# Performance work log

Hardware: AMD Instinct MI355X
Metric: run time of the kernel (lower is better)

The kernel has to match this reference:

```python
import jax, jax.numpy as jnp
import numpy as np
import math

D_MODEL = 1024
N_HEADS = 16
D_K = D_MODEL // N_HEADS
D_FF = 4096
B = 2
S = 2048
LN_EPS = 1e-3  # Keras LayerNormalization default


def setup_inputs() -> dict:
    key = jax.random.key(0)
    ks = jax.random.split(key, 16)
    s = 0.02
    inp = {
        "x": jax.random.normal(ks[0], (B, S, D_MODEL), dtype=jnp.float32),
        "weights": jax.random.uniform(ks[1], (B, S), dtype=jnp.float32),
        # attention projections (Dense: y = x @ W + b)
        "Wq": jax.random.normal(ks[2], (D_MODEL, D_MODEL), jnp.float32) * s,
        "bq": jnp.zeros((D_MODEL,), jnp.float32),
        "Wk": jax.random.normal(ks[3], (D_MODEL, D_MODEL), jnp.float32) * s,
        "bk": jnp.zeros((D_MODEL,), jnp.float32),
        "Wv": jax.random.normal(ks[4], (D_MODEL, D_MODEL), jnp.float32) * s,
        "bv": jnp.zeros((D_MODEL,), jnp.float32),
        "Wo": jax.random.normal(ks[5], (D_MODEL, D_MODEL), jnp.float32) * s,
        "bo": jnp.zeros((D_MODEL,), jnp.float32),
        # FFN
        "W1": jax.random.normal(ks[6], (D_MODEL, D_FF), jnp.float32) * s,
        "b1": jnp.zeros((D_FF,), jnp.float32),
        "W2": jax.random.normal(ks[7], (D_FF, D_MODEL), jnp.float32) * s,
        "b2": jnp.zeros((D_MODEL,), jnp.float32),
        # layer norms
        "g1": jnp.ones((D_MODEL,), jnp.float32),
        "be1": jnp.zeros((D_MODEL,), jnp.float32),
        "g2": jnp.ones((D_MODEL,), jnp.float32),
        "be2": jnp.zeros((D_MODEL,), jnp.float32),
    }
    return inp


def _layer_norm(x, gamma, beta):
    mu = jnp.mean(x, axis=-1, keepdims=True)
    var = jnp.mean(jnp.square(x - mu), axis=-1, keepdims=True)
    return (x - mu) * jax.lax.rsqrt(var + LN_EPS) * gamma + beta


def _block(x, weights, Wq, bq, Wk, bk, Wv, bv, Wo, bo, W1, b1, W2, b2, g1, be1, g2, be2):
    b, s, _ = x.shape
    # projections -> (B, H, S, d_k)
    def split_heads(y):
        return y.reshape(b, s, N_HEADS, D_K).transpose(0, 2, 1, 3)
    Q = split_heads(x @ Wq + bq)
    K = split_heads(x @ Wk + bk)
    V = split_heads(x @ Wv + bv)
    scores = jnp.einsum("bhqd,bhkd->bhqk", Q, K) / math.sqrt(D_K)
    log_w = jnp.log(weights + 1e-20)[:, None, None, :]  # (B,1,1,S)
    attn = jax.nn.softmax(scores + log_w, axis=-1)
    out = jnp.einsum("bhqk,bhkd->bhqd", attn, V)
    out = out.transpose(0, 2, 1, 3).reshape(b, s, D_MODEL)
    attn_out = out @ Wo + bo
    h = _layer_norm(x + attn_out, g1, be1)
    ffn = jax.nn.relu(h @ W1 + b1) @ W2 + b2
    return _layer_norm(h + ffn, g2, be2)


def reference(x, weights, Wq, bq, Wk, bk, Wv, bv, Wo, bo, W1, b1, W2, b2, g1, be1, g2, be2):
    return _block(x, weights, Wq, bq, Wk, bk, Wv, bv, Wo, bo, W1, b1, W2, b2, g1, be1, g2, be2)
```

## Files before the change

### kernel.cpp

```cpp
#include <hip/hip_runtime.h>
#include <cstdint>
#include <cstddef>

#define DM 1024
#define NH 16
#define DKH 64
#define DFF 4096
#define NB 2
#define SQL 2048
#define MROWS (NB * SQL)
#define QKVN 3072

typedef __attribute__((ext_vector_type(8))) __bf16 bf16x8;
typedef __attribute__((ext_vector_type(8))) short short8;
typedef __attribute__((ext_vector_type(4))) float f32x4;

__device__ __forceinline__ unsigned short f2bf(float f) {
    unsigned u = __float_as_uint(f);
    u += 0x7fffu + ((u >> 16) & 1u);
    return (unsigned short)(u >> 16);
}
__device__ __forceinline__ bf16x8 ldfrag(const unsigned short* p) {
    return __builtin_bit_cast(bf16x8, *(const short8*)p);
}
__device__ __forceinline__ void gl_lds16(const void* g, void* lds) {
    __builtin_amdgcn_global_load_lds(
        (const __attribute__((address_space(1))) unsigned int*)g,
        (__attribute__((address_space(3))) unsigned int*)lds, 16, 0, 0);
}
#define MFMA16(a, b, c) __builtin_amdgcn_mfma_f32_16x16x32_bf16(a, b, c, 0, 0, 0)

__global__ __launch_bounds__(256) void prep_misc(const float* __restrict__ x,
                                                 const float* __restrict__ wts,
                                                 const float* __restrict__ bq,
                                                 const float* __restrict__ bk,
                                                 const float* __restrict__ bv,
                                                 unsigned short* __restrict__ x_bf,
                                                 float* __restrict__ logw,
                                                 float* __restrict__ bqkv) {
    const int bid = blockIdx.x, tid = threadIdx.x;
    if (bid < 4096) {
        int i = (bid * 256 + tid) * 4;
        float4 v = *(const float4*)&x[i];
        ushort4 o;
        o.x = f2bf(v.x); o.y = f2bf(v.y); o.z = f2bf(v.z); o.w = f2bf(v.w);
        *(ushort4*)&x_bf[i] = o;
    } else if (bid < 4112) {
        int i = (bid - 4096) * 256 + tid;
        logw[i] = logf(wts[i] + 1e-20f);
    } else {
        int i = (bid - 4112) * 256 + tid;
        if (i < QKVN)
            bqkv[i] = i < 1024 ? bq[i] * 0.125f : (i < 2048 ? bk[i - 1024] : bv[i - 2048]);
    }
}

__global__ __launch_bounds__(256) void prep_weights(const float* __restrict__ Wq,
                                                    const float* __restrict__ Wk,
                                                    const float* __restrict__ Wv,
                                                    const float* __restrict__ Wo,
                                                    const float* __restrict__ W1,
                                                    const float* __restrict__ W2,
                                                    unsigned short* __restrict__ wqkv_t,
                                                    unsigned short* __restrict__ Wo_t,
                                                    unsigned short* __restrict__ W1_t,
                                                    unsigned short* __restrict__ W2_t) {
    __shared__ float tile[32][33];
    const int t = blockIdx.x;
    const float* in;
    unsigned short* out;
    int K = DM, N = DM, n0, k0;
    float scale = 1.f;
    if (t < 1024)      { in = Wq; out = wqkv_t;                      scale = 0.125f;
                         n0 = (t & 31) * 32;          k0 = (t >> 5) * 32; }
    else if (t < 2048) { in = Wk; out = wqkv_t + (size_t)1024 * DM;
                         n0 = ((t - 1024) & 31) * 32; k0 = ((t - 1024) >> 5) * 32; }
    else if (t < 3072) { in = Wv; out = wqkv_t + (size_t)2048 * DM;
                         n0 = ((t - 2048) & 31) * 32; k0 = ((t - 2048) >> 5) * 32; }
    else if (t < 4096) { in = Wo; out = Wo_t;
                         n0 = ((t - 3072) & 31) * 32; k0 = ((t - 3072) >> 5) * 32; }
    else if (t < 8192) { in = W1; out = W1_t; N = DFF;
                         n0 = ((t - 4096) & 127) * 32; k0 = ((t - 4096) >> 7) * 32; }
    else               { in = W2; out = W2_t; K = DFF;
                         n0 = ((t - 8192) & 31) * 32;  k0 = ((t - 8192) >> 5) * 32; }
    const int tx = threadIdx.x & 31, ty = threadIdx.x >> 5;
#pragma unroll
    for (int i = 0; i < 32; i += 8)
        tile[ty + i][tx] = in[(size_t)(k0 + ty + i) * N + n0 + tx];
    __syncthreads();
#pragma unroll
    for (int i = 0; i < 32; i += 8)
        out[(size_t)(n0 + ty + i) * K + k0 + tx] = f2bf(tile[tx][ty + i] * scale);
}

template <int BN, bool RELU, int OMODE, int KSPL>
__global__ __launch_bounds__(256) void gemm_kernel(const unsigned short* __restrict__ A,
                                                   const unsigned short* __restrict__ Wt,
                                                   const float* __restrict__ bias,
                                                   void* __restrict__ outp,
                                                   unsigned short* __restrict__ vtp,
                                                   int M, int N, int K) {
    constexpr int NT = BN / 32;
    __shared__ unsigned short As[128 * 64];
    __shared__ unsigned short Bs[BN * 64];
    const int tid = threadIdx.x;
    const int wave = tid >> 6, lane = tid & 63;
    const int col16 = lane & 15, quad = lane >> 4;
    const int lrow = lane >> 3, sblk = (lane & 7) ^ (lrow & 7);
    const int m0 = blockIdx.y * 128, n0 = blockIdx.x * BN;
    const int wm = (wave >> 1) * 64, wn = (wave & 1) * (BN / 2);
    const int kbeg = (KSPL > 1) ? blockIdx.z * (K / KSPL) : 0;
    const int kend = kbeg + K / KSPL;

    f32x4 acc[4][NT] = {};

    for (int k0 = kbeg; k0 < kend; k0 += 64) {
        __syncthreads();
#pragma unroll
        for (int c = wave; c < 16; c += 4)
            gl_lds16(&A[(size_t)(m0 + c * 8 + lrow) * K + k0 + sblk * 8], &As[c * 512]);
#pragma unroll
        for (int c = wave; c < BN / 8; c += 4)
            gl_lds16(&Wt[(size_t)(n0 + c * 8 + lrow) * K + k0 + sblk * 8], &Bs[c * 512]);
        __syncthreads();
#pragma unroll
        for (int kk8 = 0; kk8 < 8; kk8 += 4) {
            bf16x8 af[4], bfr[NT];
#pragma unroll
            for (int t = 0; t < 4; ++t) {
                int R = wm + t * 16 + col16;
                af[t] = ldfrag(&As[R * 64 + (((kk8 + quad) ^ (R & 7)) << 3)]);
            }
#pragma unroll
            for (int t = 0; t < NT; ++t) {
                int R = wn + t * 16 + col16;
                bfr[t] = ldfrag(&Bs[R * 64 + (((kk8 + quad) ^ (R & 7)) << 3)]);
            }
#pragma unroll
            for (int mt = 0; mt < 4; ++mt)
#pragma unroll
                for (int nt = 0; nt < NT; ++nt)
                    acc[mt][nt] = MFMA16(af[mt], bfr[nt], acc[mt][nt]);
        }
    }

    float* outf = (float*)outp + ((KSPL > 1) ? (size_t)blockIdx.z * M * N : 0);
#pragma unroll
    for (int mt = 0; mt < 4; ++mt)
#pragma unroll
        for (int nt = 0; nt < NT; ++nt) {
            int col = n0 + wn + nt * 16 + col16;
            float bv = (KSPL == 1 || blockIdx.z == 0) ? bias[col] : 0.f;
            if (OMODE == 2 && col >= 2048) {
                int dl = (col - 2048) & 63, hh = (col - 2048) >> 6;
                int row0 = m0 + wm + mt * 16 + quad * 4;
                int bb = row0 >> 11, sb = row0 & 2047;
                ushort4 w4;
                w4.x = f2bf(acc[mt][nt][0] + bv);
                w4.y = f2bf(acc[mt][nt][1] + bv);
                w4.z = f2bf(acc[mt][nt][2] + bv);
                w4.w = f2bf(acc[mt][nt][3] + bv);
                *(ushort4*)&vtp[(size_t)(bb * NH + hh) * DKH * SQL + (size_t)dl * SQL + sb] = w4;
            } else {
#pragma unroll
                for (int r = 0; r < 4; ++r) {
                    int row = m0 + wm + mt * 16 + quad * 4 + r;
                    float v = acc[mt][nt][r] + bv;
                    if (RELU) v = fmaxf(v, 0.f);
                    if (OMODE == 0)
                        outf[(size_t)row * N + col] = v;
                    else
                        ((unsigned short*)outp)[(size_t)row * N + col] = f2bf(v);
                }
            }
        }
}

__global__ __launch_bounds__(512) void flash_kernel(const unsigned short* __restrict__ qkv,
                                                    const unsigned short* __restrict__ vt,
                                                    const float* __restrict__ logw,
                                                    unsigned short* __restrict__ attn_bf) {
    __shared__ unsigned short Ks[64 * 64];
    __shared__ unsigned short Vt[64 * 64];
    __shared__ unsigned short Ps[8][16][72];
    __shared__ float lws[64];

    const int tid = threadIdx.x, wave = tid >> 6, lane = tid & 63;
    const int col16 = lane & 15, quad = lane >> 4;
    const int lrow = lane >> 3, sblk = (lane & 7) ^ (lrow & 7);
    const int bh = blockIdx.y, b = bh >> 4, h = bh & 15;
    const int q0 = blockIdx.x * 128;

    const unsigned short* Kg = qkv + (size_t)b * SQL * QKVN + 1024 + h * DKH;
    const unsigned short* Vg = vt + (size_t)bh * DKH * SQL;

    bf16x8 qf[2];
    {
        const unsigned short* qrow =
            qkv + (size_t)(b * SQL + q0 + wave * 16 + col16) * QKVN + h * DKH;
        qf[0] = ldfrag(qrow + quad * 8);
        qf[1] = ldfrag(qrow + 32 + quad * 8);
    }
    bf16x8 ones;
    {
        short8 o8 = {0x3f80, 0x3f80, 0x3f80, 0x3f80, 0x3f80, 0x3f80, 0x3f80, 0x3f80};
        ones = __builtin_bit_cast(bf16x8, o8);
    }

    f32x4 o[4] = {};
    f32x4 lacc = {};

    for (int kt = 0; kt < SQL; kt += 64) {
        __syncthreads();
        if (wave < 8) {
            int c = wave;
            gl_lds16(&Kg[(size_t)(kt + c * 8 + lrow) * QKVN + sblk * 8], &Ks[c * 512]);
            gl_lds16(&Vg[(size_t)(c * 8 + lrow) * SQL + kt + sblk * 8], &Vt[c * 512]);
        }
        if (tid < 64) lws[tid] = logw[b * SQL + kt + tid];
        __syncthreads();

        float pv[4][4];
#pragma unroll
        for (int nt = 0; nt < 4; ++nt) {
            int R = nt * 16 + col16;
            f32x4 s4 = {};
            s4 = MFMA16(qf[0], ldfrag(&Ks[R * 64 + ((quad ^ (R & 7)) << 3)]), s4);
            s4 = MFMA16(qf[1], ldfrag(&Ks[R * 64 + (((4 + quad) ^ (R & 7)) << 3)]), s4);
            float lw = lws[R];
#pragma unroll
            for (int r = 0; r < 4; ++r) pv[nt][r] = __expf(s4[r] + lw);
        }
#pragma unroll
        for (int nt = 0; nt < 4; ++nt)
#pragma unroll
            for (int r = 0; r < 4; ++r)
                Ps[wave][quad * 4 + r][nt * 16 + col16] = f2bf(pv[nt][r]);
        __syncthreads();

#pragma unroll
        for (int kk8 = 0; kk8 < 8; kk8 += 4) {
            bf16x8 psf = ldfrag(&Ps[wave][col16][(kk8 + quad) << 3]);
            lacc = MFMA16(ones, psf, lacc);
#pragma unroll
            for (int dt = 0; dt < 4; ++dt) {
                int R = dt * 16 + col16;
                bf16x8 vf = ldfrag(&Vt[R * 64 + (((kk8 + quad) ^ (R & 7)) << 3)]);
                o[dt] = MFMA16(vf, psf, o[dt]);
            }
        }
    }

    const float rl = 1.0f / lacc[0];
    const int qrow = b * SQL + q0 + wave * 16 + col16;
#pragma unroll
    for (int dt = 0; dt < 4; ++dt) {
        ushort4 h4;
        h4.x = f2bf(o[dt][0] * rl);
        h4.y = f2bf(o[dt][1] * rl);
        h4.z = f2bf(o[dt][2] * rl);
        h4.w = f2bf(o[dt][3] * rl);
        *(ushort4*)&attn_bf[(size_t)qrow * DM + h * DKH + dt * 16 + quad * 4] = h4;
    }
}

__global__ __launch_bounds__(256) void ln1_kernel(const float* __restrict__ x,
                                                  const float* __restrict__ d0,
                                                  const float* __restrict__ d1,
                                                  const float* __restrict__ g,
                                                  const float* __restrict__ be,
                                                  float* __restrict__ hf,
                                                  unsigned short* __restrict__ hb) {
    const int row = blockIdx.x, tid = threadIdx.x;
    float4 xv = *(const float4*)&x[(size_t)row * DM + tid * 4];
    float4 av = *(const float4*)&d0[(size_t)row * DM + tid * 4];
    float4 bv = *(const float4*)&d1[(size_t)row * DM + tid * 4];
    float v[4] = {xv.x + av.x + bv.x, xv.y + av.y + bv.y, xv.z + av.z + bv.z,
                  xv.w + av.w + bv.w};
    float s = v[0] + v[1] + v[2] + v[3];
    float ss = v[0] * v[0] + v[1] * v[1] + v[2] * v[2] + v[3] * v[3];
#pragma unroll
    for (int m = 1; m < 64; m <<= 1) { s += __shfl_xor(s, m); ss += __shfl_xor(ss, m); }
    __shared__ float sb[4], ssb[4];
    if ((tid & 63) == 0) { sb[tid >> 6] = s; ssb[tid >> 6] = ss; }
    __syncthreads();
    s = sb[0] + sb[1] + sb[2] + sb[3];
    ss = ssb[0] + ssb[1] + ssb[2] + ssb[3];
    float mu = s * (1.f / DM);
    float var = fmaxf(ss * (1.f / DM) - mu * mu, 0.f);
    float rs = rsqrtf(var + 1e-3f);
#pragma unroll
    for (int i = 0; i < 4; ++i) {
        int c = tid * 4 + i;
        float y = (v[i] - mu) * rs * g[c] + be[c];
        hf[(size_t)row * DM + c] = y;
        hb[(size_t)row * DM + c] = f2bf(y);
    }
}

__global__ __launch_bounds__(256) void ln2_kernel(const float* __restrict__ hf,
                                                  const float* __restrict__ d0,
                                                  const float* __restrict__ d1,
                                                  const float* __restrict__ g,
                                                  const float* __restrict__ be,
                                                  float* __restrict__ outp) {
    const int row = blockIdx.x, tid = threadIdx.x;
    float4 hv = *(const float4*)&hf[(size_t)row * DM + tid * 4];
    float4 av = *(const float4*)&d0[(size_t)row * DM + tid * 4];
    float4 bv = *(const float4*)&d1[(size_t)row * DM + tid * 4];
    float v[4] = {hv.x + av.x + bv.x, hv.y + av.y + bv.y, hv.z + av.z + bv.z,
                  hv.w + av.w + bv.w};
    float s = v[0] + v[1] + v[2] + v[3];
    float ss = v[0] * v[0] + v[1] * v[1] + v[2] * v[2] + v[3] * v[3];
#pragma unroll
    for (int m = 1; m < 64; m <<= 1) { s += __shfl_xor(s, m); ss += __shfl_xor(ss, m); }
    __shared__ float sb[4], ssb[4];
    if ((tid & 63) == 0) { sb[tid >> 6] = s; ssb[tid >> 6] = ss; }
    __syncthreads();
    s = sb[0] + sb[1] + sb[2] + sb[3];
    ss = ssb[0] + ssb[1] + ssb[2] + ssb[3];
    float mu = s * (1.f / DM);
    float var = fmaxf(ss * (1.f / DM) - mu * mu, 0.f);
    float rs = rsqrtf(var + 1e-3f);
    float4 ov;
    ov.x = (v[0] - mu) * rs * g[tid * 4 + 0] + be[tid * 4 + 0];
    ov.y = (v[1] - mu) * rs * g[tid * 4 + 1] + be[tid * 4 + 1];
    ov.z = (v[2] - mu) * rs * g[tid * 4 + 2] + be[tid * 4 + 2];
    ov.w = (v[3] - mu) * rs * g[tid * 4 + 3] + be[tid * 4 + 3];
    *(float4*)&outp[(size_t)row * DM + tid * 4] = ov;
}

extern "C" void kernel_launch(void* const* d_in, const int* in_sizes, int n_in,
                              void* d_out, int out_size, void* d_ws, size_t ws_size,
                              hipStream_t stream) {
    const float* x   = (const float*)d_in[0];
    const float* wts = (const float*)d_in[1];
    const float* Wq  = (const float*)d_in[2];
    const float* bq  = (const float*)d_in[3];
    const float* Wk  = (const float*)d_in[4];
    const float* bk  = (const float*)d_in[5];
    const float* Wv  = (const float*)d_in[6];
    const float* bv  = (const float*)d_in[7];
    const float* Wo  = (const float*)d_in[8];
    const float* bo  = (const float*)d_in[9];
    const float* W1  = (const float*)d_in[10];
    const float* b1  = (const float*)d_in[11];
    const float* W2  = (const float*)d_in[12];
    const float* b2  = (const float*)d_in[13];
    const float* g1  = (const float*)d_in[14];
    const float* be1 = (const float*)d_in[15];
    const float* g2  = (const float*)d_in[16];
    const float* be2 = (const float*)d_in[17];

    char* ws = (char*)d_ws;
    const size_t MB = 1u << 20;
    unsigned short* qkv_bf  = (unsigned short*)(ws + 0 * MB);
    unsigned short* vt      = (unsigned short*)(ws + 24 * MB);
    unsigned short* x_bf    = (unsigned short*)(ws + 32 * MB);
    unsigned short* wqkv_t  = (unsigned short*)(ws + 40 * MB);
    unsigned short* Wo_t    = (unsigned short*)(ws + 46 * MB);
    unsigned short* W1_t    = (unsigned short*)(ws + 48 * MB);
    float* h_f32            = (float*)(ws + 64 * MB);
    unsigned short* h_bf    = (unsigned short*)(ws + 80 * MB);
    unsigned short* W2_t    = (unsigned short*)(ws + 88 * MB);
    float* bqkv             = (float*)(ws + 96 * MB);
    float* logw             = (float*)(ws + 96 * MB + 0x8000);
    unsigned short* attn_bf = (unsigned short*)(ws + 32 * MB);
    float* attnproj         = (float*)(ws + 0 * MB);
    unsigned short* ffn1_bf = (unsigned short*)(ws + 0 * MB);
    float* ffn2             = (float*)(ws + 32 * MB);

    prep_misc<<<4124, 256, 0, stream>>>(x, wts, bq, bk, bv, x_bf, logw, bqkv);
    prep_weights<<<12288, 256, 0, stream>>>(Wq, Wk, Wv, Wo, W1, W2,
                                            wqkv_t, Wo_t, W1_t, W2_t);

    gemm_kernel<128, false, 2, 1><<<dim3(QKVN / 128, MROWS / 128), 256, 0, stream>>>(
        x_bf, wqkv_t, bqkv, qkv_bf, vt, MROWS, QKVN, DM);

    flash_kernel<<<dim3(SQL / 128, NB * NH), 512, 0, stream>>>(qkv_bf, vt, logw, attn_bf);

    gemm_kernel<64, false, 0, 2><<<dim3(DM / 64, MROWS / 128, 2), 256, 0, stream>>>(
        attn_bf, Wo_t, bo, attnproj, nullptr, MROWS, DM, DM);
    ln1_kernel<<<MROWS, 256, 0, stream>>>(x, attnproj, attnproj + (size_t)MROWS * DM,
                                          g1, be1, h_f32, h_bf);

    gemm_kernel<128, true, 1, 1><<<dim3(DFF / 128, MROWS / 128), 256, 0, stream>>>(
        h_bf, W1_t, b1, ffn1_bf, nullptr, MROWS, DFF, DM);
    gemm_kernel<64, false, 0, 2><<<dim3(DM / 64, MROWS / 128, 2), 256, 0, stream>>>(
        ffn1_bf, W2_t, b2, ffn2, nullptr, MROWS, DM, DFF);
    ln2_kernel<<<MROWS, 256, 0, stream>>>(h_f32, ffn2, ffn2 + (size_t)MROWS * DM,
                                          g2, be2, (float*)d_out);
}
```

Baseline: 356.7 us.

## Merge prep kernels and remap block indices for XCD-aware L2 locality

Combines the two preprocessing launches into one kernel, removing a launch and its serialization gap. Block indices in the GEMM and flash-attention kernels are remapped so that consecutive hardware-dispatched blocks (round-robined across 8 XCDs) land on tiles sharing the same weight columns or the same head. The goal is better L2 reuse per XCD. The remap assumes gridDim.x is divisible by 8 and that the flash grid has 32 heads by 16 query tiles; other shapes would break the mapping.

```diff
diff --git a/kernel.cpp b/kernel.cpp
--- a/kernel.cpp
+++ b/kernel.cpp
@@ -30,43 +30,43 @@
 }
 #define MFMA16(a, b, c) __builtin_amdgcn_mfma_f32_16x16x32_bf16(a, b, c, 0, 0, 0)
 
-__global__ __launch_bounds__(256) void prep_misc(const float* __restrict__ x,
-                                                 const float* __restrict__ wts,
-                                                 const float* __restrict__ bq,
-                                                 const float* __restrict__ bk,
-                                                 const float* __restrict__ bv,
-                                                 unsigned short* __restrict__ x_bf,
-                                                 float* __restrict__ logw,
-                                                 float* __restrict__ bqkv) {
-    const int bid = blockIdx.x, tid = threadIdx.x;
-    if (bid < 4096) {
-        int i = (bid * 256 + tid) * 4;
-        float4 v = *(const float4*)&x[i];
-        ushort4 o;
-        o.x = f2bf(v.x); o.y = f2bf(v.y); o.z = f2bf(v.z); o.w = f2bf(v.w);
-        *(ushort4*)&x_bf[i] = o;
-    } else if (bid < 4112) {
-        int i = (bid - 4096) * 256 + tid;
-        logw[i] = logf(wts[i] + 1e-20f);
-    } else {
-        int i = (bid - 4112) * 256 + tid;
-        if (i < QKVN)
-            bqkv[i] = i < 1024 ? bq[i] * 0.125f : (i < 2048 ? bk[i - 1024] : bv[i - 2048]);
-    }
-}
-
-__global__ __launch_bounds__(256) void prep_weights(const float* __restrict__ Wq,
-                                                    const float* __restrict__ Wk,
-                                                    const float* __restrict__ Wv,
-                                                    const float* __restrict__ Wo,
-                                                    const float* __restrict__ W1,
-                                                    const float* __restrict__ W2,
-                                                    unsigned short* __restrict__ wqkv_t,
-                                                    unsigned short* __restrict__ Wo_t,
-                                                    unsigned short* __restrict__ W1_t,
-                                                    unsigned short* __restrict__ W2_t) {
+__global__ __launch_bounds__(256) void prep_all(const float* __restrict__ Wq,
+                                                const float* __restrict__ Wk,
+                                                const float* __restrict__ Wv,
+                                                const float* __restrict__ Wo,
+                                                const float* __restrict__ W1,
+                                                const float* __restrict__ W2,
+                                                const float* __restrict__ x,
+                                                const float* __restrict__ wts,
+                                                const float* __restrict__ bq,
+                                                const float* __restrict__ bk,
+                                                const float* __restrict__ bv,
+                                                unsigned short* __restrict__ wqkv_t,
+                                                unsigned short* __restrict__ Wo_t,
+                                                unsigned short* __restrict__ W1_t,
+                                                unsigned short* __restrict__ W2_t,
+                                                unsigned short* __restrict__ x_bf,
+                                                float* __restrict__ logw,
+                                                float* __restrict__ bqkv) {
+    const int t = blockIdx.x, tid = threadIdx.x;
+    if (t >= 12288) {
+        if (t < 16384) {
+            int i = ((t - 12288) * 256 + tid) * 4;
+            float4 v = *(const float4*)&x[i];
+            ushort4 o;
+            o.x = f2bf(v.x); o.y = f2bf(v.y); o.z = f2bf(v.z); o.w = f2bf(v.w);
+            *(ushort4*)&x_bf[i] = o;
+        } else if (t < 16400) {
+            int i = (t - 16384) * 256 + tid;
+            logw[i] = logf(wts[i] + 1e-20f);
+        } else {
+            int i = (t - 16400) * 256 + tid;
+            if (i < QKVN)
+                bqkv[i] = i < 1024 ? bq[i] * 0.125f : (i < 2048 ? bk[i - 1024] : bv[i - 2048]);
+        }
+        return;
+    }
     __shared__ float tile[32][33];
-    const int t = blockIdx.x;
     const float* in;
     unsigned short* out;
     int K = DM, N = DM, n0, k0;
@@ -107,7 +107,11 @@
     const int wave = tid >> 6, lane = tid & 63;
     const int col16 = lane & 15, quad = lane >> 4;
     const int lrow = lane >> 3, sblk = (lane & 7) ^ (lrow & 7);
-    const int m0 = blockIdx.y * 128, n0 = blockIdx.x * BN;
+    const int f = blockIdx.y * gridDim.x + blockIdx.x;
+    const int nper = gridDim.x >> 3;
+    const int bx = (f & 7) * nper + (f >> 3) % nper;
+    const int by = (f >> 3) / nper;
+    const int m0 = by * 128, n0 = bx * BN;
     const int wm = (wave >> 1) * 64, wn = (wave & 1) * (BN / 2);
     const int kbeg = (KSPL > 1) ? blockIdx.z * (K / KSPL) : 0;
     const int kend = kbeg + K / KSPL;
@@ -188,8 +192,11 @@
     const int tid = threadIdx.x, wave = tid >> 6, lane = tid & 63;
     const int col16 = lane & 15, quad = lane >> 4;
     const int lrow = lane >> 3, sblk = (lane & 7) ^ (lrow & 7);
-    const int bh = blockIdx.y, b = bh >> 4, h = bh & 15;
-    const int q0 = blockIdx.x * 128;
+    const int f = blockIdx.y * gridDim.x + blockIdx.x;
+    const int g = f >> 3;
+    const int bh = (f & 7) * 4 + (g & 3);
+    const int q0 = (g >> 2) * 128;
+    const int b = bh >> 4, h = bh & 15;
 
     const unsigned short* Kg = qkv + (size_t)b * SQL * QKVN + 1024 + h * DKH;
     const unsigned short* Vg = vt + (size_t)bh * DKH * SQL;
@@ -370,9 +377,8 @@
     unsigned short* ffn1_bf = (unsigned short*)(ws + 0 * MB);
     float* ffn2             = (float*)(ws + 32 * MB);
 
-    prep_misc<<<4124, 256, 0, stream>>>(x, wts, bq, bk, bv, x_bf, logw, bqkv);
-    prep_weights<<<12288, 256, 0, stream>>>(Wq, Wk, Wv, Wo, W1, W2,
-                                            wqkv_t, Wo_t, W1_t, W2_t);
+    prep_all<<<16412, 256, 0, stream>>>(Wq, Wk, Wv, Wo, W1, W2, x, wts, bq, bk, bv,
+                                        wqkv_t, Wo_t, W1_t, W2_t, x_bf, logw, bqkv);
 
     gemm_kernel<128, false, 2, 1><<<dim3(QKVN / 128, MROWS / 128), 256, 0, stream>>>(
         x_bf, wqkv_t, bqkv, qkv_bf, vt, MROWS, QKVN, DM);
```

New measurement: 346.7 us. -2.8%, faster.
